# Performance work log

Hardware: AMD Instinct MI355X
Metric: run time of the kernel (lower is better)

The kernel has to match this reference:

```python
import jax, jax.numpy as jnp
import numpy as np

B, S, D, H, F, E = 8, 1024, 1024, 16, 3584, 2
HD = D // H
NUM_LABELS = 2
EPS = 1e-6


def setup_inputs() -> dict:
    key = jax.random.key(0)
    ks = jax.random.split(key, 10)
    w = lambda k, shape: jax.random.normal(k, shape, jnp.float32) * 0.02
    return {
        "hidden_states": jax.random.normal(ks[0], (B, S, D), jnp.float32),
        "ln1_w": jnp.ones((D,), jnp.float32),
        "q_w": w(ks[1], (D, D)),
        "k_w": w(ks[2], (D, D)),
        "v_w": w(ks[3], (D, D)),
        "o_w": w(ks[4], (D, D)),
        "ln2_w": jnp.ones((D,), jnp.float32),
        "router_w": w(ks[5], (D, E)),
        "gate_w": w(ks[6], (E, D, F)),
        "up_w": w(ks[7], (E, D, F)),
        "down_w": w(ks[8], (E, F, D)),
        "final_ln_w": jnp.ones((D,), jnp.float32),
        "score_w": w(ks[9], (D, NUM_LABELS)),
    }


def rmsnorm(x, w):
    var = jnp.mean(jnp.square(x), axis=-1, keepdims=True)
    return x * jax.lax.rsqrt(var + EPS) * w


def reference(hidden_states, ln1_w, q_w, k_w, v_w, o_w, ln2_w, router_w,
              gate_w, up_w, down_w, final_ln_w, score_w):
    x = hidden_states  # [B,S,D]
    # --- attention block (Jamba attention: no RoPE, no bias, causal) ---
    res = x
    h = rmsnorm(x, ln1_w)
    q = (h @ q_w).reshape(B, S, H, HD).transpose(0, 2, 1, 3)  # [B,H,S,HD]
    k = (h @ k_w).reshape(B, S, H, HD).transpose(0, 2, 1, 3)
    v = (h @ v_w).reshape(B, S, H, HD).transpose(0, 2, 1, 3)
    scores = jnp.einsum("bhqd,bhkd->bhqk", q, k) / np.sqrt(HD).astype(np.float32)
    causal = jnp.tril(jnp.ones((S, S), bool))
    scores = jnp.where(causal, scores, jnp.finfo(jnp.float32).min)
    attn = jax.nn.softmax(scores, axis=-1)
    ctx = jnp.einsum("bhqk,bhkd->bhqd", attn, v)
    attn_out = ctx.transpose(0, 2, 1, 3).reshape(B, S, D) @ o_w
    x = res + attn_out
    # --- top-1 MoE FFN (Jamba: softmax router, top-k, NO renormalization) ---
    res = x
    h = rmsnorm(x, ln2_w).reshape(B * S, D)
    router_logits = h @ router_w  # [N,E]
    probs = jax.nn.softmax(router_logits.astype(jnp.float32), axis=-1)
    top_w = jnp.max(probs, axis=-1)       # top-1 weight
    sel = jnp.argmax(probs, axis=-1)      # selected expert id
    moe = jnp.zeros_like(h)
    for e in range(E):  # fixed tiny loop over experts
        y = (jax.nn.silu(h @ gate_w[e]) * (h @ up_w[e])) @ down_w[e]
        moe = moe + jnp.where(sel == e, top_w, 0.0)[:, None] * y
    x = res + moe.reshape(B, S, D)
    # --- final RMSNorm + score head on first token ---
    x = rmsnorm(x, final_ln_w)
    logits = x[:, 0, :] @ score_w  # [B, NUM_LABELS]
    return logits
```

## Files before the change

kernel.cpp:

```cpp
#include <hip/hip_runtime.h>
#include <math.h>

#define B 8
#define S 1024
#define D 1024
#define F 3584

#define KSV 32
#define KSG 16
#define KSD 56
#define CH32 32
#define CHG 64
#define CHD 64

#define LD4(p) (*(const float4*)(p))
#define FMA4(A, s, W) { (A).x += (s)*(W).x; (A).y += (s)*(W).y; (A).z += (s)*(W).z; (A).w += (s)*(W).w; }

#define BB8(bb, ACC, XS, CH, koff) { \
  float4 xa = LD4((XS) + (bb)*(CH) + (koff)); \
  float4 xb = LD4((XS) + (bb)*(CH) + (koff) + 4); \
  FMA4(ACC, xa.x, w0); FMA4(ACC, xa.y, w1); FMA4(ACC, xa.z, w2); FMA4(ACC, xa.w, w3); \
  FMA4(ACC, xb.x, w4); FMA4(ACC, xb.y, w5); FMA4(ACC, xb.z, w6); FMA4(ACC, xb.w, w7); }

#define ALL8(XS, CH, koff) \
  BB8(0, acc0, XS, CH, koff) BB8(1, acc1, XS, CH, koff) \
  BB8(2, acc2, XS, CH, koff) BB8(3, acc3, XS, CH, koff) \
  BB8(4, acc4, XS, CH, koff) BB8(5, acc5, XS, CH, koff) \
  BB8(6, acc6, XS, CH, koff) BB8(7, acc7, XS, CH, koff)

#define DECL_ACC \
  float4 acc0 = {0,0,0,0}, acc1 = {0,0,0,0}, acc2 = {0,0,0,0}, acc3 = {0,0,0,0}; \
  float4 acc4 = {0,0,0,0}, acc5 = {0,0,0,0}, acc6 = {0,0,0,0}, acc7 = {0,0,0,0};

#define PREFETCH_LOOP(XS, CH, ST) \
  float4 w0 = Wp[0*(ST)], w1 = Wp[1*(ST)], w2 = Wp[2*(ST)], w3 = Wp[3*(ST)]; \
  float4 w4 = Wp[4*(ST)], w5 = Wp[5*(ST)], w6 = Wp[6*(ST)], w7 = Wp[7*(ST)]; \
  Wp += 8 * (ST); \
  _Pragma("unroll") \
  for (int t = 0; t < (CH) / 8 - 1; t++) { \
    float4 n0 = Wp[0*(ST)], n1 = Wp[1*(ST)], n2 = Wp[2*(ST)], n3 = Wp[3*(ST)]; \
    float4 n4 = Wp[4*(ST)], n5 = Wp[5*(ST)], n6 = Wp[6*(ST)], n7 = Wp[7*(ST)]; \
    Wp += 8 * (ST); \
    ALL8(XS, CH, t * 8); \
    w0 = n0; w1 = n1; w2 = n2; w3 = n3; w4 = n4; w5 = n5; w6 = n6; w7 = n7; \
  } \
  ALL8(XS, CH, (CH) - 8);

__device__ __forceinline__ float block_sum256(float v, volatile float* buf) {
  #pragma unroll
  for (int o = 32; o; o >>= 1) v += __shfl_down(v, o);
  __syncthreads();
  if ((threadIdx.x & 63) == 0) buf[threadIdx.x >> 6] = v;
  __syncthreads();
  return buf[0] + buf[1] + buf[2] + buf[3];
}

__global__ void k_rms1(const float* __restrict__ hs, const float* __restrict__ w,
                       float* __restrict__ h1) {
  __shared__ float buf[4];
  int b = blockIdx.x;
  int idx = threadIdx.x * 4;
  float4 x = LD4(hs + (size_t)b * S * D + idx);
  float ss = x.x * x.x + x.y * x.y + x.z * x.z + x.w * x.w;
  float tot = block_sum256(ss, buf);
  float sc = rsqrtf(tot * (1.f / (float)D) + 1e-6f);
  float4 wv = LD4(w + idx);
  float4 o;
  o.x = x.x * sc * wv.x; o.y = x.y * sc * wv.y;
  o.z = x.z * sc * wv.z; o.w = x.w * sc * wv.w;
  *(float4*)(h1 + b * D + idx) = o;
}

__global__ __launch_bounds__(256, 2) void k_mvp(const float* __restrict__ X,
                                                const float* __restrict__ W,
                                                float* __restrict__ P) {
  __shared__ float xs[8 * CH32];
  int i0 = blockIdx.x * CH32;
  xs[threadIdx.x] = X[(threadIdx.x >> 5) * D + i0 + (threadIdx.x & 31)];
  __syncthreads();
  int j = threadIdx.x * 4;
  const float4* Wp = (const float4*)(W + (size_t)i0 * D + j);
  const int st = D / 4;
  DECL_ACC
  PREFETCH_LOOP(xs, CH32, st)
  #define MV_ST(bb, ACC) *(float4*)(P + ((size_t)blockIdx.x * 8 + (bb)) * D + j) = ACC;
  MV_ST(0, acc0) MV_ST(1, acc1) MV_ST(2, acc2) MV_ST(3, acc3)
  MV_ST(4, acc4) MV_ST(5, acc5) MV_ST(6, acc6) MV_ST(7, acc7)
  #undef MV_ST
}

__global__ __launch_bounds__(256, 2) void k_mvp_red(const float* __restrict__ Vp,
                                                    const float* __restrict__ W,
                                                    float* __restrict__ P) {
  __shared__ float xs[8 * CH32];
  int i0 = blockIdx.x * CH32;
  {
    int bb = threadIdx.x >> 5, k = threadIdx.x & 31;
    float s = 0.f;
    #pragma unroll 8
    for (int p = 0; p < KSV; p++)
      s += Vp[((size_t)p * 8 + bb) * D + i0 + k];
    xs[threadIdx.x] = s;
  }
  __syncthreads();
  int j = threadIdx.x * 4;
  const float4* Wp = (const float4*)(W + (size_t)i0 * D + j);
  const int st = D / 4;
  DECL_ACC
  PREFETCH_LOOP(xs, CH32, st)
  #define MV_ST(bb, ACC) *(float4*)(P + ((size_t)blockIdx.x * 8 + (bb)) * D + j) = ACC;
  MV_ST(0, acc0) MV_ST(1, acc1) MV_ST(2, acc2) MV_ST(3, acc3)
  MV_ST(4, acc4) MV_ST(5, acc5) MV_ST(6, acc6) MV_ST(7, acc7)
  #undef MV_ST
}

__global__ void k_mid(const float* __restrict__ hs, const float* __restrict__ Op,
                      const float* __restrict__ ln2, const float* __restrict__ rw,
                      float* __restrict__ xr, float* __restrict__ h2,
                      float* __restrict__ topw, int* __restrict__ sel) {
  __shared__ float buf[4];
  int b = blockIdx.x;
  int idx = threadIdx.x * 4;
  float4 x = LD4(hs + (size_t)b * S * D + idx);
  #pragma unroll 8
  for (int p = 0; p < KSV; p++) {
    float4 v = LD4(Op + ((size_t)p * 8 + b) * D + idx);
    x.x += v.x; x.y += v.y; x.z += v.z; x.w += v.w;
  }
  *(float4*)(xr + b * D + idx) = x;
  float ss = x.x * x.x + x.y * x.y + x.z * x.z + x.w * x.w;
  float tot = block_sum256(ss, buf);
  float sc = rsqrtf(tot * (1.f / (float)D) + 1e-6f);
  float4 wv = LD4(ln2 + idx);
  float4 h;
  h.x = x.x * sc * wv.x; h.y = x.y * sc * wv.y;
  h.z = x.z * sc * wv.z; h.w = x.w * sc * wv.w;
  *(float4*)(h2 + b * D + idx) = h;
  float r0 = h.x * rw[idx * 2] + h.y * rw[(idx + 1) * 2] +
             h.z * rw[(idx + 2) * 2] + h.w * rw[(idx + 3) * 2];
  float r1 = h.x * rw[idx * 2 + 1] + h.y * rw[(idx + 1) * 2 + 1] +
             h.z * rw[(idx + 2) * 2 + 1] + h.w * rw[(idx + 3) * 2 + 1];
  r0 = block_sum256(r0, buf);
  r1 = block_sum256(r1, buf);
  if (threadIdx.x == 0) {
    float m = fmaxf(r0, r1);
    float e0 = __expf(r0 - m), e1 = __expf(r1 - m);
    float inv = 1.f / (e0 + e1);
    float p0 = e0 * inv, p1 = e1 * inv;
    topw[b] = fmaxf(p0, p1);
    sel[b] = (p1 > p0) ? 1 : 0;
  }
}

__global__ __launch_bounds__(256, 2) void k_gateup(const float* __restrict__ h2,
                                                   const float* __restrict__ gw,
                                                   const float* __restrict__ uw,
                                                   float* __restrict__ Pgu) {
  __shared__ float xs[8 * CHG];
  int i0 = blockIdx.y * CHG;
  {
    int t = threadIdx.x, t2 = threadIdx.x + 256;
    xs[t]  = h2[(t >> 6) * D + i0 + (t & 63)];
    xs[t2] = h2[(t2 >> 6) * D + i0 + (t2 & 63)];
  }
  __syncthreads();
  int c = blockIdx.x * 1024 + threadIdx.x * 4;
  int m = c / F;
  int j = c - m * F;
  const float* base = (m < 2 ? gw : uw) + (size_t)(m & 1) * D * F;
  const float4* Wp = (const float4*)(base + (size_t)i0 * F + j);
  const int st = F / 4;
  DECL_ACC
  PREFETCH_LOOP(xs, CHG, st)
  #define GU_ST(bb, ACC) \
    *(float4*)(Pgu + (((size_t)blockIdx.y * 4 + m) * 8 + (bb)) * F + j) = ACC;
  GU_ST(0, acc0) GU_ST(1, acc1) GU_ST(2, acc2) GU_ST(3, acc3)
  GU_ST(4, acc4) GU_ST(5, acc5) GU_ST(6, acc6) GU_ST(7, acc7)
  #undef GU_ST
}

__global__ __launch_bounds__(256, 2) void k_down(const float* __restrict__ Pgu,
                                                 const float* __restrict__ dw,
                                                 float* __restrict__ Dp) {
  __shared__ float xs[8 * CHD];
  int e = blockIdx.x;
  int i0 = blockIdx.y * CHD;
  #pragma unroll
  for (int t = threadIdx.x; t < 8 * CHD; t += 256) {
    int bb = t >> 6, k = t & 63;
    float gs = 0.f, us = 0.f;
    #pragma unroll 8
    for (int kc = 0; kc < KSG; kc++) {
      gs += Pgu[(((size_t)kc * 4 + e)     * 8 + bb) * F + i0 + k];
      us += Pgu[(((size_t)kc * 4 + 2 + e) * 8 + bb) * F + i0 + k];
    }
    xs[t] = (gs / (1.f + __expf(-gs))) * us;
  }
  __syncthreads();
  int j = threadIdx.x * 4;
  const float4* Wp = (const float4*)(dw + (size_t)e * F * D + (size_t)i0 * D + j);
  const int st = D / 4;
  DECL_ACC
  PREFETCH_LOOP(xs, CHD, st)
  #define DN_ST(bb, ACC) \
    *(float4*)(Dp + (((size_t)blockIdx.y * 2 + e) * 8 + (bb)) * D + j) = ACC;
  DN_ST(0, acc0) DN_ST(1, acc1) DN_ST(2, acc2) DN_ST(3, acc3)
  DN_ST(4, acc4) DN_ST(5, acc5) DN_ST(6, acc6) DN_ST(7, acc7)
  #undef DN_ST
}

__global__ void k_final(const float* __restrict__ xr, const float* __restrict__ Dp,
                        const float* __restrict__ topw, const int* __restrict__ sel,
                        const float* __restrict__ flw, const float* __restrict__ sw,
                        float* __restrict__ out) {
  __shared__ float buf[4];
  int b = blockIdx.x;
  int e = sel[b];
  float tw = topw[b];
  int idx = threadIdx.x * 4;
  float4 y = {0,0,0,0};
  #pragma unroll 8
  for (int p = 0; p < KSD; p++) {
    float4 v = LD4(Dp + (((size_t)p * 2 + e) * 8 + b) * D + idx);
    y.x += v.x; y.y += v.y; y.z += v.z; y.w += v.w;
  }
  float4 x = LD4(xr + b * D + idx);
  x.x += tw * y.x; x.y += tw * y.y; x.z += tw * y.z; x.w += tw * y.w;
  float ss = x.x * x.x + x.y * x.y + x.z * x.z + x.w * x.w;
  float tot = block_sum256(ss, buf);
  float sc = rsqrtf(tot * (1.f / (float)D) + 1e-6f);
  float4 wv = LD4(flw + idx);
  float n0 = x.x * sc * wv.x, n1 = x.y * sc * wv.y;
  float n2 = x.z * sc * wv.z, n3 = x.w * sc * wv.w;
  float l0 = n0 * sw[idx * 2] + n1 * sw[(idx + 1) * 2] +
             n2 * sw[(idx + 2) * 2] + n3 * sw[(idx + 3) * 2];
  float l1 = n0 * sw[idx * 2 + 1] + n1 * sw[(idx + 1) * 2 + 1] +
             n2 * sw[(idx + 2) * 2 + 1] + n3 * sw[(idx + 3) * 2 + 1];
  l0 = block_sum256(l0, buf);
  l1 = block_sum256(l1, buf);
  if (threadIdx.x == 0) { out[b * 2 + 0] = l0; out[b * 2 + 1] = l1; }
}

extern "C" void kernel_launch(void* const* d_in, const int* in_sizes, int n_in,
                              void* d_out, int out_size, void* d_ws, size_t ws_size,
                              hipStream_t stream) {
  const float* hs  = (const float*)d_in[0];
  const float* ln1 = (const float*)d_in[1];
  const float* vw  = (const float*)d_in[4];
  const float* ow  = (const float*)d_in[5];
  const float* ln2 = (const float*)d_in[6];
  const float* rw  = (const float*)d_in[7];
  const float* gw  = (const float*)d_in[8];
  const float* uw  = (const float*)d_in[9];
  const float* dw  = (const float*)d_in[10];
  const float* flw = (const float*)d_in[11];
  const float* sw  = (const float*)d_in[12];

  float* ws = (float*)d_ws;
  float* h1   = ws;
  float* Vp   = ws + 8192;
  float* Op   = ws + 270336;
  float* xr   = ws + 532480;
  float* h2   = ws + 540672;
  float* Pgu  = ws + 548864;
  float* Dp   = ws + 2383872;
  float* topw = ws + 3301376;
  int*   sel  = (int*)(ws + 3301384);

  k_rms1<<<8, 256, 0, stream>>>(hs, ln1, h1);
  k_mvp<<<KSV, 256, 0, stream>>>(h1, vw, Vp);
  k_mvp_red<<<KSV, 256, 0, stream>>>(Vp, ow, Op);
  k_mid<<<8, 256, 0, stream>>>(hs, Op, ln2, rw, xr, h2, topw, sel);
  k_gateup<<<dim3(14, KSG), 256, 0, stream>>>(h2, gw, uw, Pgu);
  k_down<<<dim3(2, KSD), 256, 0, stream>>>(Pgu, dw, Dp);
  k_final<<<8, 256, 0, stream>>>(xr, Dp, topw, sel, flw, sw, (float*)d_out);
}
```

Baseline: 220.9 us.

## Fuse RMSNorm into V projection, double split-K blocks, separate SiLU reduction

The first RMSNorm is folded into the V-projection kernel: each block recomputes the per-row norm scale, which removes one launch. The split-K factors for the V/O, gate/up and down matvecs are doubled, with halved chunk sizes, so more blocks run in parallel on the bandwidth-bound weight streaming. The SiLU-gating reduction over gate/up partials moves out of k_down into a separate vectorised kernel, so each down block no longer redundantly re-reduces the partials. The cost is more partial-sum traffic, one extra launch, and redundant norm computation in every V block.

```diff
diff --git a/kernel.cpp b/kernel.cpp
--- a/kernel.cpp
+++ b/kernel.cpp
@@ -6,12 +6,11 @@
 #define D 1024
 #define F 3584
 
-#define KSV 32
-#define KSG 16
-#define KSD 56
+#define KSV 64
+#define CHV 16
+#define KSG 32
+#define KSD 112
 #define CH32 32
-#define CHG 64
-#define CHD 64
 
 #define LD4(p) (*(const float4*)(p))
 #define FMA4(A, s, W) { (A).x += (s)*(W).x; (A).y += (s)*(W).y; (A).z += (s)*(W).z; (A).w += (s)*(W).w; }
@@ -55,59 +54,73 @@
   return buf[0] + buf[1] + buf[2] + buf[3];
 }
 
-__global__ void k_rms1(const float* __restrict__ hs, const float* __restrict__ w,
-                       float* __restrict__ h1) {
-  __shared__ float buf[4];
-  int b = blockIdx.x;
-  int idx = threadIdx.x * 4;
-  float4 x = LD4(hs + (size_t)b * S * D + idx);
-  float ss = x.x * x.x + x.y * x.y + x.z * x.z + x.w * x.w;
-  float tot = block_sum256(ss, buf);
-  float sc = rsqrtf(tot * (1.f / (float)D) + 1e-6f);
-  float4 wv = LD4(w + idx);
-  float4 o;
-  o.x = x.x * sc * wv.x; o.y = x.y * sc * wv.y;
-  o.z = x.z * sc * wv.z; o.w = x.w * sc * wv.w;
-  *(float4*)(h1 + b * D + idx) = o;
-}
-
-__global__ __launch_bounds__(256, 2) void k_mvp(const float* __restrict__ X,
-                                                const float* __restrict__ W,
-                                                float* __restrict__ P) {
-  __shared__ float xs[8 * CH32];
-  int i0 = blockIdx.x * CH32;
-  xs[threadIdx.x] = X[(threadIdx.x >> 5) * D + i0 + (threadIdx.x & 31)];
+__global__ __launch_bounds__(256, 2) void k_v(const float* __restrict__ hs,
+                                              const float* __restrict__ ln1,
+                                              const float* __restrict__ W,
+                                              float* __restrict__ P) {
+  __shared__ float sq[256];
+  __shared__ float scale[8];
+  __shared__ float xs[8 * CHV];
+  int i0 = blockIdx.x * CHV;
+  {
+    int b = threadIdx.x >> 5, l = threadIdx.x & 31;
+    const float* xrow = hs + (size_t)b * S * D + l * 32;
+    float ss = 0.f;
+    #pragma unroll
+    for (int u = 0; u < 8; u++) {
+      float4 v = LD4(xrow + u * 4);
+      ss += v.x * v.x + v.y * v.y + v.z * v.z + v.w * v.w;
+    }
+    sq[threadIdx.x] = ss;
+  }
+  __syncthreads();
+  if (threadIdx.x < 8) {
+    float s = 0.f;
+    #pragma unroll
+    for (int u = 0; u < 32; u++) s += sq[threadIdx.x * 32 + u];
+    scale[threadIdx.x] = rsqrtf(s * (1.f / (float)D) + 1e-6f);
+  }
+  __syncthreads();
+  if (threadIdx.x < 8 * CHV) {
+    int bb = threadIdx.x >> 4, k = threadIdx.x & 15;
+    xs[threadIdx.x] = hs[(size_t)bb * S * D + i0 + k] * scale[bb] * ln1[i0 + k];
+  }
   __syncthreads();
   int j = threadIdx.x * 4;
   const float4* Wp = (const float4*)(W + (size_t)i0 * D + j);
   const int st = D / 4;
   DECL_ACC
-  PREFETCH_LOOP(xs, CH32, st)
+  PREFETCH_LOOP(xs, CHV, st)
   #define MV_ST(bb, ACC) *(float4*)(P + ((size_t)blockIdx.x * 8 + (bb)) * D + j) = ACC;
   MV_ST(0, acc0) MV_ST(1, acc1) MV_ST(2, acc2) MV_ST(3, acc3)
   MV_ST(4, acc4) MV_ST(5, acc5) MV_ST(6, acc6) MV_ST(7, acc7)
   #undef MV_ST
 }
 
-__global__ __launch_bounds__(256, 2) void k_mvp_red(const float* __restrict__ Vp,
-                                                    const float* __restrict__ W,
-                                                    float* __restrict__ P) {
-  __shared__ float xs[8 * CH32];
-  int i0 = blockIdx.x * CH32;
-  {
-    int bb = threadIdx.x >> 5, k = threadIdx.x & 31;
-    float s = 0.f;
-    #pragma unroll 8
-    for (int p = 0; p < KSV; p++)
-      s += Vp[((size_t)p * 8 + bb) * D + i0 + k];
-    xs[threadIdx.x] = s;
+__global__ __launch_bounds__(256, 2) void k_o(const float* __restrict__ Vp,
+                                              const float* __restrict__ W,
+                                              float* __restrict__ P) {
+  __shared__ float xs[8 * CHV];
+  int i0 = blockIdx.x * CHV;
+  if (threadIdx.x < 8 * CHV) {
+    int bb = threadIdx.x >> 4, k = threadIdx.x & 15;
+    const float* src = Vp + (size_t)bb * D + i0 + k;
+    float s0 = 0.f, s1 = 0.f, s2 = 0.f, s3 = 0.f;
+    #pragma unroll 4
+    for (int p = 0; p < KSV; p += 4) {
+      s0 += src[(size_t)(p + 0) * 8 * D];
+      s1 += src[(size_t)(p + 1) * 8 * D];
+      s2 += src[(size_t)(p + 2) * 8 * D];
+      s3 += src[(size_t)(p + 3) * 8 * D];
+    }
+    xs[threadIdx.x] = (s0 + s1) + (s2 + s3);
   }
   __syncthreads();
   int j = threadIdx.x * 4;
   const float4* Wp = (const float4*)(W + (size_t)i0 * D + j);
   const int st = D / 4;
   DECL_ACC
-  PREFETCH_LOOP(xs, CH32, st)
+  PREFETCH_LOOP(xs, CHV, st)
   #define MV_ST(bb, ACC) *(float4*)(P + ((size_t)blockIdx.x * 8 + (bb)) * D + j) = ACC;
   MV_ST(0, acc0) MV_ST(1, acc1) MV_ST(2, acc2) MV_ST(3, acc3)
   MV_ST(4, acc4) MV_ST(5, acc5) MV_ST(6, acc6) MV_ST(7, acc7)
@@ -156,13 +169,9 @@
                                                    const float* __restrict__ gw,
                                                    const float* __restrict__ uw,
                                                    float* __restrict__ Pgu) {
-  __shared__ float xs[8 * CHG];
-  int i0 = blockIdx.y * CHG;
-  {
-    int t = threadIdx.x, t2 = threadIdx.x + 256;
-    xs[t]  = h2[(t >> 6) * D + i0 + (t & 63)];
-    xs[t2] = h2[(t2 >> 6) * D + i0 + (t2 & 63)];
-  }
+  __shared__ float xs[8 * CH32];
+  int i0 = blockIdx.y * CH32;
+  xs[threadIdx.x] = h2[(threadIdx.x >> 5) * D + i0 + (threadIdx.x & 31)];
   __syncthreads();
   int c = blockIdx.x * 1024 + threadIdx.x * 4;
   int m = c / F;
@@ -171,7 +180,7 @@
   const float4* Wp = (const float4*)(base + (size_t)i0 * F + j);
   const int st = F / 4;
   DECL_ACC
-  PREFETCH_LOOP(xs, CHG, st)
+  PREFETCH_LOOP(xs, CH32, st)
   #define GU_ST(bb, ACC) \
     *(float4*)(Pgu + (((size_t)blockIdx.y * 4 + m) * 8 + (bb)) * F + j) = ACC;
   GU_ST(0, acc0) GU_ST(1, acc1) GU_ST(2, acc2) GU_ST(3, acc3)
@@ -179,29 +188,40 @@
   #undef GU_ST
 }
 
-__global__ __launch_bounds__(256, 2) void k_down(const float* __restrict__ Pgu,
+__global__ void k_silu_red(const float* __restrict__ Pgu, float* __restrict__ g) {
+  int o = blockIdx.x * 256 + threadIdx.x;
+  int e = o / (8 * F / 4);
+  int rem = o - e * (8 * F / 4);
+  const float4* P4 = (const float4*)Pgu;
+  float4 ga = {0,0,0,0}, ua = {0,0,0,0};
+  #pragma unroll 8
+  for (int kc = 0; kc < KSG; kc++) {
+    float4 gv = P4[(size_t)(kc * 4 + e)     * (8 * F / 4) + rem];
+    float4 uv = P4[(size_t)(kc * 4 + 2 + e) * (8 * F / 4) + rem];
+    ga.x += gv.x; ga.y += gv.y; ga.z += gv.z; ga.w += gv.w;
+    ua.x += uv.x; ua.y += uv.y; ua.z += uv.z; ua.w += uv.w;
+  }
+  float4 r;
+  r.x = (ga.x / (1.f + __expf(-ga.x))) * ua.x;
+  r.y = (ga.y / (1.f + __expf(-ga.y))) * ua.y;
+  r.z = (ga.z / (1.f + __expf(-ga.z))) * ua.z;
+  r.w = (ga.w / (1.f + __expf(-ga.w))) * ua.w;
+  ((float4*)g)[o] = r;
+}
+
+__global__ __launch_bounds__(256, 2) void k_down(const float* __restrict__ g,
                                                  const float* __restrict__ dw,
                                                  float* __restrict__ Dp) {
-  __shared__ float xs[8 * CHD];
+  __shared__ float xs[8 * CH32];
   int e = blockIdx.x;
-  int i0 = blockIdx.y * CHD;
-  #pragma unroll
-  for (int t = threadIdx.x; t < 8 * CHD; t += 256) {
-    int bb = t >> 6, k = t & 63;
-    float gs = 0.f, us = 0.f;
-    #pragma unroll 8
-    for (int kc = 0; kc < KSG; kc++) {
-      gs += Pgu[(((size_t)kc * 4 + e)     * 8 + bb) * F + i0 + k];
-      us += Pgu[(((size_t)kc * 4 + 2 + e) * 8 + bb) * F + i0 + k];
-    }
-    xs[t] = (gs / (1.f + __expf(-gs))) * us;
-  }
+  int i0 = blockIdx.y * CH32;
+  xs[threadIdx.x] = g[(size_t)e * 8 * F + (threadIdx.x >> 5) * F + i0 + (threadIdx.x & 31)];
   __syncthreads();
   int j = threadIdx.x * 4;
   const float4* Wp = (const float4*)(dw + (size_t)e * F * D + (size_t)i0 * D + j);
   const int st = D / 4;
   DECL_ACC
-  PREFETCH_LOOP(xs, CHD, st)
+  PREFETCH_LOOP(xs, CH32, st)
   #define DN_ST(bb, ACC) \
     *(float4*)(Dp + (((size_t)blockIdx.y * 2 + e) * 8 + (bb)) * D + j) = ACC;
   DN_ST(0, acc0) DN_ST(1, acc1) DN_ST(2, acc2) DN_ST(3, acc3)
@@ -257,21 +277,21 @@
   const float* sw  = (const float*)d_in[12];
 
   float* ws = (float*)d_ws;
-  float* h1   = ws;
-  float* Vp   = ws + 8192;
-  float* Op   = ws + 270336;
-  float* xr   = ws + 532480;
-  float* h2   = ws + 540672;
-  float* Pgu  = ws + 548864;
-  float* Dp   = ws + 2383872;
-  float* topw = ws + 3301376;
-  int*   sel  = (int*)(ws + 3301384);
-
-  k_rms1<<<8, 256, 0, stream>>>(hs, ln1, h1);
-  k_mvp<<<KSV, 256, 0, stream>>>(h1, vw, Vp);
-  k_mvp_red<<<KSV, 256, 0, stream>>>(Vp, ow, Op);
+  float* Vp   = ws;
+  float* Op   = ws + 524288;
+  float* xr   = ws + 1048576;
+  float* h2   = ws + 1056768;
+  float* Pgu  = ws + 1064960;
+  float* g    = ws + 4734976;
+  float* Dp   = ws + 4792320;
+  float* topw = ws + 6627328;
+  int*   sel  = (int*)(ws + 6627336);
+
+  k_v<<<KSV, 256, 0, stream>>>(hs, ln1, vw, Vp);
+  k_o<<<KSV, 256, 0, stream>>>(Vp, ow, Op);
   k_mid<<<8, 256, 0, stream>>>(hs, Op, ln2, rw, xr, h2, topw, sel);
   k_gateup<<<dim3(14, KSG), 256, 0, stream>>>(h2, gw, uw, Pgu);
-  k_down<<<dim3(2, KSD), 256, 0, stream>>>(Pgu, dw, Dp);
+  k_silu_red<<<56, 256, 0, stream>>>(Pgu, g);
+  k_down<<<dim3(2, KSD), 256, 0, stream>>>(g, dw, Dp);
   k_final<<<8, 256, 0, stream>>>(xr, Dp, topw, sel, flw, sw, (float*)d_out);
 }
```

Result: faster. 206.6 us (-6.5%).
